# Performance work log

Measured on AMD Instinct MI355X. Metric: run time of the kernel, lower is better.

## Reference

```python
import jax, jax.numpy as jnp
import numpy as np
from jax.scipy.special import logsumexp

B, N = 256, 65536
NEG_INF = jnp.float32(-1e30)  # acts as -inf for logsumexp, keeps grads finite


def setup_inputs() -> dict:
    key = jax.random.key(0)
    k1, k2 = jax.random.split(key)
    sim = jax.random.uniform(k1, (B, N), dtype=jnp.float32)
    label = jax.random.uniform(k2, (B, N), dtype=jnp.float32)
    return {"sim": sim, "label": label}


def _ranking_loss(sim, label):
    m = 0.2
    gamma = 64.0
    delta_p = 1.0 - m  # 0.8
    delta_n = m        # 0.2

    pos_mask = label > 0.5
    neg_mask = label < 0.25

    # ---- positives: logit_p = -relu(0.8 - sim).detach() * (sim - 0.8) * gamma ----
    alpha_p = jax.lax.stop_gradient(jnp.maximum(0.8 - sim, 0.0))
    logit_p = -alpha_p * (sim - delta_p) * gamma
    lse_p = logsumexp(jnp.where(pos_mask, logit_p, NEG_INF), axis=1)
    # torch fallback: no positives -> logit_p = [0.0], logsumexp == 0
    lse_p = jnp.where(pos_mask.any(axis=1), lse_p, 0.0)

    # ---- negatives: if >20 negatives, keep only top-10 largest sims ----
    alpha_n_all = jax.lax.stop_gradient(jnp.maximum(sim - 0.2, 0.0))
    logit_n_all = alpha_n_all * (sim - delta_n) * gamma
    lse_n_all = logsumexp(jnp.where(neg_mask, logit_n_all, NEG_INF), axis=1)

    neg_sim_masked = jnp.where(neg_mask, sim, NEG_INF)
    top_v, _ = jax.lax.top_k(neg_sim_masked, 10)  # [B, 10]
    alpha_n_top = jax.lax.stop_gradient(jnp.maximum(top_v - 0.2, 0.0))
    logit_n_top = alpha_n_top * (top_v - delta_n) * gamma
    lse_n_top = logsumexp(logit_n_top, axis=1)

    n_neg = neg_mask.sum(axis=1)
    lse_n = jnp.where(n_neg > 20, lse_n_top, lse_n_all)

    loss_loc = jax.nn.softplus(lse_n + lse_p).sum()
    return loss_loc / sim.shape[0]  # reduction='mean'


def reference(sim, label):
    return _ranking_loss(sim, label)
```

## Files before the change

### kernel.cpp

```cpp
#include <hip/hip_runtime.h>
#include <cmath>

#define NEG_INF (-1.0e30f)

static constexpr int B = 256;
static constexpr int N = 65536;
static constexpr int THREADS = 256;
static constexpr int SPLIT = 4;
static constexpr float C_OFF = 40.96f;

__device__ __forceinline__ float wave_sum_f(float v) {
#pragma unroll
  for (int off = 32; off >= 1; off >>= 1) v += __shfl_xor(v, off, 64);
  return v;
}
__device__ __forceinline__ int wave_sum_i(int v) {
#pragma unroll
  for (int off = 32; off >= 1; off >>= 1) v += __shfl_xor(v, off, 64);
  return v;
}

__device__ __forceinline__ void merge_lists_shfl(float t[16], int off) {
  float b[16];
#pragma unroll
  for (int i = 0; i < 16; ++i) b[i] = __shfl_xor(t[i], off, 64);
  float c[16];
#pragma unroll
  for (int i = 0; i < 16; ++i) c[i] = fmaxf(t[i], b[15 - i]);
#pragma unroll
  for (int s = 8; s >= 1; s >>= 1) {
#pragma unroll
    for (int i = 0; i < 16; ++i) {
      if ((i & s) == 0) {
        float lo = c[i], hi = c[i + s];
        c[i] = fmaxf(lo, hi);
        c[i + s] = fminf(lo, hi);
      }
    }
  }
#pragma unroll
  for (int i = 0; i < 16; ++i) t[i] = c[i];
}

__device__ __forceinline__ void merge_lists_local(float a[16], const float b[16]) {
  float c[16];
#pragma unroll
  for (int i = 0; i < 16; ++i) c[i] = fmaxf(a[i], b[15 - i]);
#pragma unroll
  for (int s = 8; s >= 1; s >>= 1) {
#pragma unroll
    for (int i = 0; i < 16; ++i) {
      if ((i & s) == 0) {
        float lo = c[i], hi = c[i + s];
        c[i] = fmaxf(lo, hi);
        c[i + s] = fminf(lo, hi);
      }
    }
  }
#pragma unroll
  for (int i = 0; i < 16; ++i) a[i] = c[i];
}

__device__ __forceinline__ void process_elem(float s, float l, float& s_p,
                                             float& s_n, int& nn, float t[16]) {
  const bool pos = l > 0.5f;
  const bool neg = l < 0.25f;
  float d = pos ? (0.8f - s) : (s - 0.2f);
  float r = fmaxf(d, 0.f);
  float arg = __builtin_fmaf(64.f * r, r, -C_OFF);
  float e = __expf(arg);
  if (pos) s_p += e;
  if (neg) {
    s_n += e;
    ++nn;
    if (s > t[9]) {
      t[9] = s;
#pragma unroll
      for (int i = 9; i > 0; --i) {
        float a = t[i - 1], bb = t[i];
        t[i - 1] = fmaxf(a, bb);
        t[i] = fminf(a, bb);
      }
    }
  }
}

__global__ void __launch_bounds__(THREADS, 4) ranking_partial_kernel(
    const float* __restrict__ sim, const float* __restrict__ label,
    float* __restrict__ ws_sp, float* __restrict__ ws_sn,
    int* __restrict__ ws_cnt, float* __restrict__ ws_top) {
  const int blk = blockIdx.x;
  const int row = blk >> 2;
  const int part = blk & 3;
  const int tid = threadIdx.x;
  const size_t base4 = (size_t)row * (N / 4) + (size_t)part * (N / (4 * SPLIT));
  const float4* sim4 = reinterpret_cast<const float4*>(sim) + base4;
  const float4* lab4 = reinterpret_cast<const float4*>(label) + base4;

  float s_p = 0.f, s_n = 0.f;
  int nn = 0;
  float t[16];
#pragma unroll
  for (int i = 0; i < 16; ++i) t[i] = NEG_INF;

  constexpr int ITER = N / 4 / THREADS / SPLIT;
#pragma unroll
  for (int it = 0; it < ITER; it += 4) {
    float4 sv[4], lv[4];
#pragma unroll
    for (int j = 0; j < 4; ++j) {
      sv[j] = sim4[(it + j) * THREADS + tid];
      lv[j] = lab4[(it + j) * THREADS + tid];
    }
#pragma unroll
    for (int j = 0; j < 4; ++j) {
      process_elem(sv[j].x, lv[j].x, s_p, s_n, nn, t);
      process_elem(sv[j].y, lv[j].y, s_p, s_n, nn, t);
      process_elem(sv[j].z, lv[j].z, s_p, s_n, nn, t);
      process_elem(sv[j].w, lv[j].w, s_p, s_n, nn, t);
    }
  }

  s_p = wave_sum_f(s_p);
  s_n = wave_sum_f(s_n);
  nn = wave_sum_i(nn);
#pragma unroll
  for (int off = 1; off < 64; off <<= 1) merge_lists_shfl(t, off);

  __shared__ float ls_p[4], ls_n[4];
  __shared__ int ls_c[4];
  __shared__ float ltop[4][16];
  const int wave = tid >> 6, lane = tid & 63;
  if (lane == 0) {
    ls_p[wave] = s_p;
    ls_n[wave] = s_n;
    ls_c[wave] = nn;
#pragma unroll
    for (int i = 0; i < 16; ++i) ltop[wave][i] = t[i];
  }
  __syncthreads();

  if (wave == 0) {
    float m[16];
    if (lane < 4) {
#pragma unroll
      for (int i = 0; i < 16; ++i) m[i] = ltop[lane][i];
    } else {
#pragma unroll
      for (int i = 0; i < 16; ++i) m[i] = NEG_INF;
    }
    merge_lists_shfl(m, 1);
    merge_lists_shfl(m, 2);

    float sp = (lane < 4) ? ls_p[lane] : 0.f;
    float sn = (lane < 4) ? ls_n[lane] : 0.f;
    int cn = (lane < 4) ? ls_c[lane] : 0;
    sp = wave_sum_f(sp);
    sn = wave_sum_f(sn);
    cn = wave_sum_i(cn);

    if (lane == 0) {
      ws_sp[blk] = sp;
      ws_sn[blk] = sn;
      ws_cnt[blk] = cn;
#pragma unroll
      for (int i = 0; i < 16; ++i) ws_top[blk * 16 + i] = m[i];
    }
  }
}

__global__ void __launch_bounds__(256) combine_kernel(
    const float* __restrict__ ws_sp, const float* __restrict__ ws_sn,
    const int* __restrict__ ws_cnt, const float* __restrict__ ws_top,
    float* __restrict__ out) {
  const int r = threadIdx.x;
  const int p0 = r * SPLIT;

  float a[16];
#pragma unroll
  for (int i = 0; i < 16; ++i) a[i] = ws_top[p0 * 16 + i];
#pragma unroll
  for (int k = 1; k < SPLIT; ++k) {
    float b[16];
#pragma unroll
    for (int i = 0; i < 16; ++i) b[i] = ws_top[(p0 + k) * 16 + i];
    merge_lists_local(a, b);
  }

  float sp = 0.f, sn = 0.f;
  int cn = 0;
#pragma unroll
  for (int k = 0; k < SPLIT; ++k) {
    sp += ws_sp[p0 + k];
    sn += ws_sn[p0 + k];
    cn += ws_cnt[p0 + k];
  }

  float lse_p = (sp > 0.f) ? (C_OFF + __logf(sp)) : 0.f;
  float lse_n_all = (sn > 0.f) ? (C_OFF + __logf(sn)) : NEG_INF;

  float mx = NEG_INF;
  float lg[10];
#pragma unroll
  for (int i = 0; i < 10; ++i) {
    float v = a[i];
    float al = fmaxf(v - 0.2f, 0.f);
    float lo = al * (v - 0.2f) * 64.f;
    lg[i] = lo;
    mx = fmaxf(mx, lo);
  }
  float ss = 0.f;
#pragma unroll
  for (int i = 0; i < 10; ++i) ss += __expf(lg[i] - mx);
  float lse_n_top = mx + __logf(ss);

  float lse_n = (cn > 20) ? lse_n_top : lse_n_all;
  float x = lse_n + lse_p;
  float loss = fmaxf(x, 0.f) + log1pf(__expf(-fabsf(x)));

  float v = wave_sum_f(loss);
  __shared__ float wsh[4];
  if ((r & 63) == 0) wsh[r >> 6] = v;
  __syncthreads();
  if (r == 0) out[0] = (wsh[0] + wsh[1] + wsh[2] + wsh[3]) * (1.0f / 256.0f);
}

extern "C" void kernel_launch(void* const* d_in, const int* in_sizes, int n_in,
                              void* d_out, int out_size, void* d_ws, size_t ws_size,
                              hipStream_t stream) {
  const float* sim = (const float*)d_in[0];
  const float* label = (const float*)d_in[1];
  float* out = (float*)d_out;

  constexpr int P = B * SPLIT;
  float* wsf = (float*)d_ws;
  float* ws_sp = wsf;
  float* ws_sn = wsf + P;
  float* ws_top = wsf + 2 * P;
  int* ws_cnt = (int*)(wsf + 2 * P + P * 16);

  ranking_partial_kernel<<<dim3(P), dim3(THREADS), 0, stream>>>(
      sim, label, ws_sp, ws_sn, ws_cnt, ws_top);
  combine_kernel<<<dim3(1), dim3(256), 0, stream>>>(ws_sp, ws_sn, ws_cnt, ws_top,
                                                    out);
}
```

Baseline: 161.5 us.

## Shrink per-thread top-k state, ballot-count negatives, and raise row split and occupancy

```diff
diff --git a/kernel.cpp b/kernel.cpp
--- a/kernel.cpp
+++ b/kernel.cpp
@@ -6,15 +6,10 @@
 static constexpr int B = 256;
 static constexpr int N = 65536;
 static constexpr int THREADS = 256;
-static constexpr int SPLIT = 4;
 static constexpr float C_OFF = 40.96f;
+static constexpr float PAD = 0.2f;
 
 __device__ __forceinline__ float wave_sum_f(float v) {
-#pragma unroll
-  for (int off = 32; off >= 1; off >>= 1) v += __shfl_xor(v, off, 64);
-  return v;
-}
-__device__ __forceinline__ int wave_sum_i(int v) {
 #pragma unroll
   for (int off = 32; off >= 1; off >>= 1) v += __shfl_xor(v, off, 64);
   return v;
@@ -62,7 +57,7 @@
 }
 
 __device__ __forceinline__ void process_elem(float s, float l, float& s_p,
-                                             float& s_n, int& nn, float t[16]) {
+                                             float& s_n, int& nn, float t[10]) {
   const bool pos = l > 0.5f;
   const bool neg = l < 0.25f;
   float d = pos ? (0.8f - s) : (s - 0.2f);
@@ -70,28 +65,27 @@
   float arg = __builtin_fmaf(64.f * r, r, -C_OFF);
   float e = __expf(arg);
   if (pos) s_p += e;
-  if (neg) {
-    s_n += e;
-    ++nn;
-    if (s > t[9]) {
-      t[9] = s;
-#pragma unroll
-      for (int i = 9; i > 0; --i) {
-        float a = t[i - 1], bb = t[i];
-        t[i - 1] = fmaxf(a, bb);
-        t[i] = fminf(a, bb);
-      }
-    }
-  }
-}
-
-__global__ void __launch_bounds__(THREADS, 4) ranking_partial_kernel(
+  if (neg) s_n += e;
+  nn += (int)__popcll(__ballot(neg));
+  if (neg & (s > t[9])) {
+    t[9] = s;
+#pragma unroll
+    for (int i = 9; i > 0; --i) {
+      float a = t[i - 1], bb = t[i];
+      t[i - 1] = fmaxf(a, bb);
+      t[i] = fminf(a, bb);
+    }
+  }
+}
+
+template <int SPLIT>
+__global__ void __launch_bounds__(THREADS, 8) ranking_partial_kernel(
     const float* __restrict__ sim, const float* __restrict__ label,
     float* __restrict__ ws_sp, float* __restrict__ ws_sn,
     int* __restrict__ ws_cnt, float* __restrict__ ws_top) {
   const int blk = blockIdx.x;
-  const int row = blk >> 2;
-  const int part = blk & 3;
+  const int row = blk / SPLIT;
+  const int part = blk % SPLIT;
   const int tid = threadIdx.x;
   const size_t base4 = (size_t)row * (N / 4) + (size_t)part * (N / (4 * SPLIT));
   const float4* sim4 = reinterpret_cast<const float4*>(sim) + base4;
@@ -99,9 +93,9 @@
 
   float s_p = 0.f, s_n = 0.f;
   int nn = 0;
-  float t[16];
-#pragma unroll
-  for (int i = 0; i < 16; ++i) t[i] = NEG_INF;
+  float t[10];
+#pragma unroll
+  for (int i = 0; i < 10; ++i) t[i] = PAD;
 
   constexpr int ITER = N / 4 / THREADS / SPLIT;
 #pragma unroll
@@ -121,11 +115,16 @@
     }
   }
 
+  float tl[16];
+#pragma unroll
+  for (int i = 0; i < 10; ++i) tl[i] = t[i];
+#pragma unroll
+  for (int i = 10; i < 16; ++i) tl[i] = PAD;
+
   s_p = wave_sum_f(s_p);
   s_n = wave_sum_f(s_n);
-  nn = wave_sum_i(nn);
-#pragma unroll
-  for (int off = 1; off < 64; off <<= 1) merge_lists_shfl(t, off);
+#pragma unroll
+  for (int off = 1; off < 64; off <<= 1) merge_lists_shfl(tl, off);
 
   __shared__ float ls_p[4], ls_n[4];
   __shared__ int ls_c[4];
@@ -136,7 +135,7 @@
     ls_n[wave] = s_n;
     ls_c[wave] = nn;
 #pragma unroll
-    for (int i = 0; i < 16; ++i) ltop[wave][i] = t[i];
+    for (int i = 0; i < 16; ++i) ltop[wave][i] = tl[i];
   }
   __syncthreads();
 
@@ -147,7 +146,7 @@
       for (int i = 0; i < 16; ++i) m[i] = ltop[lane][i];
     } else {
 #pragma unroll
-      for (int i = 0; i < 16; ++i) m[i] = NEG_INF;
+      for (int i = 0; i < 16; ++i) m[i] = PAD;
     }
     merge_lists_shfl(m, 1);
     merge_lists_shfl(m, 2);
@@ -157,7 +156,8 @@
     int cn = (lane < 4) ? ls_c[lane] : 0;
     sp = wave_sum_f(sp);
     sn = wave_sum_f(sn);
-    cn = wave_sum_i(cn);
+#pragma unroll
+    for (int off = 32; off >= 1; off >>= 1) cn += __shfl_xor(cn, off, 64);
 
     if (lane == 0) {
       ws_sp[blk] = sp;
@@ -169,6 +169,7 @@
   }
 }
 
+template <int SPLIT>
 __global__ void __launch_bounds__(256) combine_kernel(
     const float* __restrict__ ws_sp, const float* __restrict__ ws_sn,
     const int* __restrict__ ws_cnt, const float* __restrict__ ws_top,
@@ -225,22 +226,34 @@
   if (r == 0) out[0] = (wsh[0] + wsh[1] + wsh[2] + wsh[3]) * (1.0f / 256.0f);
 }
 
+template <int SPLIT>
+static void launch_all(const float* sim, const float* label, float* out,
+                       float* wsf, hipStream_t stream) {
+  constexpr int P = B * SPLIT;
+  float* ws_sp = wsf;
+  float* ws_sn = wsf + P;
+  float* ws_top = wsf + 2 * P;
+  int* ws_cnt = (int*)(wsf + 2 * P + P * 16);
+  ranking_partial_kernel<SPLIT><<<dim3(P), dim3(THREADS), 0, stream>>>(
+      sim, label, ws_sp, ws_sn, ws_cnt, ws_top);
+  combine_kernel<SPLIT><<<dim3(1), dim3(256), 0, stream>>>(ws_sp, ws_sn, ws_cnt,
+                                                           ws_top, out);
+}
+
 extern "C" void kernel_launch(void* const* d_in, const int* in_sizes, int n_in,
                               void* d_out, int out_size, void* d_ws, size_t ws_size,
                               hipStream_t stream) {
   const float* sim = (const float*)d_in[0];
   const float* label = (const float*)d_in[1];
   float* out = (float*)d_out;
-
-  constexpr int P = B * SPLIT;
   float* wsf = (float*)d_ws;
-  float* ws_sp = wsf;
-  float* ws_sn = wsf + P;
-  float* ws_top = wsf + 2 * P;
-  int* ws_cnt = (int*)(wsf + 2 * P + P * 16);
-
-  ranking_partial_kernel<<<dim3(P), dim3(THREADS), 0, stream>>>(
-      sim, label, ws_sp, ws_sn, ws_cnt, ws_top);
-  combine_kernel<<<dim3(1), dim3(256), 0, stream>>>(ws_sp, ws_sn, ws_cnt, ws_top,
-                                                    out);
-}
+
+  auto need = [](int split) { return (size_t)B * split * 19 * sizeof(float); };
+  if (ws_size >= need(8)) {
+    launch_all<8>(sim, label, out, wsf, stream);
+  } else if (ws_size >= need(4)) {
+    launch_all<4>(sim, label, out, wsf, stream);
+  } else {
+    launch_all<2>(sim, label, out, wsf, stream);
+  }
+}
```

Result: slower. 205.0 us (+26.9%).
